# Kernel optimization log

Measured on AMD Instinct MI355X. Metric: run time of the kernel, lower is better.

The kernel has to match this reference:

```python
import jax, jax.numpy as jnp
import numpy as np

B, S, T = 1024, 1024, 16


def setup_inputs() -> dict:
    key = jax.random.key(0)
    k1, k2, k3, k4, k5 = jax.random.split(key, 5)
    emissions = jax.random.normal(k1, (B, S, T), dtype=jnp.float32)
    tags = jax.random.randint(k2, (B, S), 0, T, dtype=jnp.int64)
    mask = jnp.ones((B, S), dtype=bool)
    # parameters (original uses uniform(-0.1, 0.1) init)
    transitions = jax.random.uniform(k3, (T, T), minval=-0.1, maxval=0.1, dtype=jnp.float32)
    start_transitions = jax.random.uniform(k4, (T,), minval=-0.1, maxval=0.1, dtype=jnp.float32)
    end_transitions = jax.random.uniform(k5, (T,), minval=-0.1, maxval=0.1, dtype=jnp.float32)
    return {
        "emissions": emissions,
        "tags": tags,
        "mask": mask,
        "transitions": transitions,
        "start_transitions": start_transitions,
        "end_transitions": end_transitions,
    }


def _forward_algorithm(emissions, mask, transitions, start_transitions, end_transitions):
    # emissions: [B,S,T], mask: [B,S] bool -> log partition [B]
    score0 = start_transitions + emissions[:, 0]  # [B,T]

    def step(score, xs):
        em_t, m_t = xs  # em_t: [B,T], m_t: [B]
        # next[b,i,j] = score[b,i] + transitions[i,j] + em_t[b,j]
        nxt = score[:, :, None] + transitions[None, :, :] + em_t[:, None, :]
        nxt = jax.nn.logsumexp(nxt, axis=1)  # over previous tag i
        score = jnp.where(m_t[:, None], nxt, score)
        return score, None

    em_rest = jnp.swapaxes(emissions[:, 1:], 0, 1)  # [S-1,B,T]
    m_rest = jnp.swapaxes(mask[:, 1:], 0, 1)        # [S-1,B]
    score, _ = jax.lax.scan(step, score0, (em_rest, m_rest))
    score = score + end_transitions
    return jax.nn.logsumexp(score, axis=1)


def _score_sentence(emissions, tags, mask, transitions, start_transitions, end_transitions):
    # gold-path score, vectorized over time. [B]
    bidx = jnp.arange(emissions.shape[0])
    score = start_transitions[tags[:, 0]] + emissions[:, 0][bidx, tags[:, 0]]
    # per-step emission scores [B,S]
    emit = jnp.take_along_axis(emissions, tags[:, :, None], axis=2)[:, :, 0]
    # NOTE: faithful to original: transitions[tags[t], tags[t-1]]
    trans = transitions[tags[:, 1:], tags[:, :-1]]  # [B,S-1]
    m = mask[:, 1:].astype(emissions.dtype)
    score = score + jnp.sum((emit[:, 1:] + trans) * m, axis=1)
    last_idx = jnp.sum(mask.astype(jnp.int32), axis=1) - 1  # [B]
    last_tags = jnp.take_along_axis(tags, last_idx[:, None].astype(tags.dtype), axis=1)[:, 0]
    score = score + end_transitions[last_tags]
    return score


def reference(emissions, tags, mask, transitions, start_transitions, end_transitions):
    emissions = emissions.astype(jnp.float32)
    gold = _score_sentence(emissions, tags, mask, transitions, start_transitions, end_transitions)
    logZ = _forward_algorithm(emissions, mask, transitions, start_transitions, end_transitions)
    nll = logZ - gold
    return jnp.mean(nll)
```

## Files before the change

kernel.cpp:

```cpp
#include <hip/hip_runtime.h>
#include <stdint.h>


#define BB 1024
#define SS 1024
#define TT 16
#define WPB 8
#define TL  128
#define RS  16
#define MS  20
#define OFFLN2 3.29244911f

typedef float    f32x4 __attribute__((ext_vector_type(4)));
typedef float    f32x2 __attribute__((ext_vector_type(2)));
typedef int      i32x4 __attribute__((ext_vector_type(4)));
typedef short    s16x4 __attribute__((ext_vector_type(4)));
typedef uint32_t u32x2 __attribute__((ext_vector_type(2)));

__device__ __forceinline__ uint32_t pkt(float lo, float hi) {
    return __builtin_amdgcn_perm(__float_as_uint(hi), __float_as_uint(lo), 0x07060302u);
}
__device__ __forceinline__ s16x4 mk_frag(uint32_t lo, uint32_t hi) {
    u32x2 t; t.x = lo; t.y = hi;
    return __builtin_bit_cast(s16x4, t);
}

__global__ __launch_bounds__(512, 4) void crf_fused(
        const float* __restrict__ em,
        const float* __restrict__ trans,
        const int*   __restrict__ tags,
        const float* __restrict__ startt,
        const float* __restrict__ endt,
        float* __restrict__ part)
{
    __shared__ __align__(16) float xbuf[WPB][TL * RS];
    __shared__ __align__(16) int   scb [WPB][16];
    __shared__ float gpart[WPB];

    const int w    = threadIdx.x >> 6;
    const int lane = threadIdx.x & 63;
    const int b    = blockIdx.x;
    const int q    = lane >> 4;
    const int m    = lane & 15;

    const float comp = 1.00390625f;
    f32x2 e01, e23;
    e01.x = __expf(trans[(4*q + 0) * TT + m]) * comp;
    e01.y = __expf(trans[(4*q + 1) * TT + m]) * comp;
    e23.x = __expf(trans[(4*q + 2) * TT + m]) * comp;
    e23.y = __expf(trans[(4*q + 3) * TT + m]) * comp;
    const s16x4 eA = mk_frag(pkt(e01.x, e01.y), pkt(e23.x, e23.y));

    const float* ep = em + (size_t)b * SS * TT + (size_t)w * TL * TT + lane;
    float* xt = xbuf[w];
    #pragma unroll
    for (int h = 0; h < 2; ++h) {
        float v[16];
        #pragma unroll
        for (int k = 0; k < 16; ++k) v[k] = ep[(h * 16 + k) * 64];
        #pragma unroll
        for (int k = 0; k < 16; ++k) xt[(4 * (h * 16 + k) + q) * RS + m] = __expf(v[k] - OFFLN2);
    }

    {
        const int t0  = w * TL + lane;
        const int t1  = t0 + 64;
        const int tg0 = tags[b * SS + t0];
        const int tg1 = tags[b * SS + t1];
        float g0 = em[((size_t)b * SS + t0) * TT + tg0];
        float g1 = em[((size_t)b * SS + t1) * TT + tg1];
        g0 += (t0 > 0) ? trans[tg0 * TT + tags[b * SS + t0 - 1]] : startt[tg0];
        g1 += trans[tg1 * TT + tags[b * SS + t1 - 1]];
        if (t1 == SS - 1) g1 += endt[tg1];
        float gs = g0 + g1;
        #pragma unroll
        for (int s2 = 1; s2 < 64; s2 <<= 1) gs += __shfl_xor(gs, s2, 64);
        if (lane == 0) gpart[w] = gs;
    }

    f32x4 sd0, sd1;
    sd0[0] = sd1[0] = (4*q + 0 == m) ? 1.f : 0.f;
    sd0[1] = sd1[1] = (4*q + 1 == m) ? 1.f : 0.f;
    sd0[2] = sd1[2] = (4*q + 2 == m) ? 1.f : 0.f;
    sd0[3] = sd1[3] = (4*q + 3 == m) ? 1.f : 0.f;
    const f32x4 zero = {0.f, 0.f, 0.f, 0.f};
    const bool skip0 = (w == 0);

#define RESCALE(sd, sc) {                                                   \
        float mx = fmaxf(fmaxf(sd[0], sd[1]), fmaxf(sd[2], sd[3]));         \
        mx = fmaxf(mx, __shfl_xor(mx, 16, 64));                             \
        mx = fmaxf(mx, __shfl_xor(mx, 32, 64));                             \
        const int e_ = (int)(__float_as_uint(mx) >> 23) - 127;              \
        const float sf_ = __uint_as_float((uint32_t)(127 - e_) << 23);      \
        sd[0] *= sf_; sd[1] *= sf_; sd[2] *= sf_; sd[3] *= sf_;             \
        sc += e_; }

    const float* xr0 = xt + 4 * q;
    const float* xr1 = xt + 64 * RS + 4 * q;
    f32x4 c0[4], c1[4];
    #pragma unroll
    for (int i = 0; i < 4; ++i) {
        c0[i] = *(const f32x4*)(xr0 + i * RS);
        c1[i] = *(const f32x4*)(xr1 + i * RS);
    }

    #pragma unroll
    for (int g = 0; g < 16; ++g) {
        f32x4 n0[4], n1[4];
        if (g < 15) {
            #pragma unroll
            for (int i = 0; i < 4; ++i) {
                n0[i] = *(const f32x4*)(xr0 + (4 * (g + 1) + i) * RS);
                n1[i] = *(const f32x4*)(xr1 + (4 * (g + 1) + i) * RS);
            }
        }
        #pragma unroll
        for (int i = 0; i < 4; ++i) {
            if (!(skip0 && g == 0 && i == 0)) {
                const s16x4 b0 = mk_frag(pkt(sd0[0], sd0[1]), pkt(sd0[2], sd0[3]));
                sd0 = __builtin_amdgcn_mfma_f32_16x16x16bf16_1k(eA, b0, zero, 0, 0, 0);
                sd0 *= c0[i];
            }
            const s16x4 b1 = mk_frag(pkt(sd1[0], sd1[1]), pkt(sd1[2], sd1[3]));
            sd1 = __builtin_amdgcn_mfma_f32_16x16x16bf16_1k(eA, b1, zero, 0, 0, 0);
            sd1 *= c1[i];
        }
        #pragma unroll
        for (int i = 0; i < 4; ++i) { c0[i] = n0[i]; c1[i] = n1[i]; }
    }

    xt[(4*q + 0) * TT + m] = sd1[0];
    xt[(4*q + 1) * TT + m] = sd1[1];
    xt[(4*q + 2) * TT + m] = sd1[2];
    xt[(4*q + 3) * TT + m] = sd1[3];
    const f32x4 at = *(const f32x4*)(xt + m * TT + 4 * q);
    const s16x4 bfm = mk_frag(pkt(sd0[0], sd0[1]), pkt(sd0[2], sd0[3]));
    const s16x4 afm = mk_frag(pkt(at.x, at.y), pkt(at.z, at.w));
    f32x4 sdw = __builtin_amdgcn_mfma_f32_16x16x16bf16_1k(afm, bfm, zero, 0, 0, 0);
    int scw = 0;
    RESCALE(sdw, scw);

    xt[(4*q + 0) * MS + m] = sdw[0];
    xt[(4*q + 1) * MS + m] = sdw[1];
    xt[(4*q + 2) * MS + m] = sdw[2];
    xt[(4*q + 3) * MS + m] = sdw[3];
    if (q == 0) scb[w][m] = scw;
    __syncthreads();

    f32x4 d = zero; int sig = 0;
    #pragma unroll
    for (int lev = 0; lev < 3; ++lev) {
        const int nact = 4 >> lev;
        if (w < nact) {
            const int iA = (2 * w + 1) << lev;
            const int iB = (2 * w) << lev;
            const float* xA = xbuf[iA];
            float*       xB = xbuf[iB];
            const f32x4 a  = *(const f32x4*)(xA + m * MS + 4 * q);
            const i32x4 s4 = *(const i32x4*)(&scb[iA][4 * q]);
            const int   sB = scb[iB][m];
            int smax = max(max(s4.x, s4.y), max(s4.z, s4.w));
            smax = max(smax, __shfl_xor(smax, 16, 64));
            smax = max(smax, __shfl_xor(smax, 32, 64));
            const float bb0 = xB[(4*q + 0) * MS + m];
            const float bb1 = xB[(4*q + 1) * MS + m];
            const float bb2 = xB[(4*q + 2) * MS + m];
            const float bb3 = xB[(4*q + 3) * MS + m];
            const float u0 = ldexpf(bb0, s4.x - smax);
            const float u1 = ldexpf(bb1, s4.y - smax);
            const float u2 = ldexpf(bb2, s4.z - smax);
            const float u3 = ldexpf(bb3, s4.w - smax);
            const s16x4 bfr = mk_frag(pkt(u0, u1), pkt(u2, u3));
            const s16x4 afr = mk_frag(pkt(a.x, a.y), pkt(a.z, a.w));
            f32x4 dd = __builtin_amdgcn_mfma_f32_16x16x16bf16_1k(afr, bfr, zero, 0, 0, 0);
            int sc_ = sB + smax;
            RESCALE(dd, sc_);
            if (lev == 2) { d = dd; sig = sc_; }
            else {
                xB[(4*q + 0) * MS + m] = dd[0];
                xB[(4*q + 1) * MS + m] = dd[1];
                xB[(4*q + 2) * MS + m] = dd[2];
                xB[(4*q + 3) * MS + m] = dd[3];
                if (q == 0) scb[iB][m] = sc_;
            }
        }
        if (lev < 2) __syncthreads();
    }
#undef RESCALE

    if (w == 0) {
        const float s0 = startt[m] + em[(size_t)b * SS * TT + m];
        float mx0 = s0;
        #pragma unroll
        for (int s2 = 1; s2 < 16; s2 <<= 1) mx0 = fmaxf(mx0, __shfl_xor(mx0, s2, 64));
        const float u0n = __expf(s0 - mx0);
        int sigmax = sig;
        #pragma unroll
        for (int s2 = 1; s2 < 16; s2 <<= 1) sigmax = max(sigmax, __shfl_xor(sigmax, s2, 64));
        const float wt = ldexpf(u0n, sig - sigmax);
        f32x4 v;
        v[0] = d[0] * wt; v[1] = d[1] * wt; v[2] = d[2] * wt; v[3] = d[3] * wt;
        #pragma unroll
        for (int s2 = 1; s2 < 16; s2 <<= 1) {
            v[0] += __shfl_xor(v[0], s2, 64);
            v[1] += __shfl_xor(v[1], s2, 64);
            v[2] += __shfl_xor(v[2], s2, 64);
            v[3] += __shfl_xor(v[3], s2, 64);
        }
        const f32x4 ee = *(const f32x4*)(endt + 4 * q);
        float z = __expf(ee.x) * v[0] + __expf(ee.y) * v[1]
                + __expf(ee.z) * v[2] + __expf(ee.w) * v[3];
        z += __shfl_xor(z, 16, 64);
        z += __shfl_xor(z, 32, 64);
        if (lane == 0) {
            float gb = 0.f;
            #pragma unroll
            for (int i = 0; i < WPB; ++i) gb += gpart[i];
            part[b] = mx0 + 0.69314718055994531f * (float)sigmax
                    + 1023.0f * OFFLN2 + __logf(z) - gb;
        }
    }
}

__global__ __launch_bounds__(256) void reduce_kernel(const float* __restrict__ part,
                                                     float* __restrict__ out)
{
    __shared__ float red[256];
    const int tid = threadIdx.x;
    float s = 0.f;
    #pragma unroll
    for (int i = 0; i < 4; ++i) s += part[tid + 256 * i];
    red[tid] = s;
    __syncthreads();
    for (int k = 128; k > 0; k >>= 1) {
        if (tid < k) red[tid] += red[tid + k];
        __syncthreads();
    }
    if (tid == 0) out[0] = red[0] * (1.0f / BB);
}

extern "C" void kernel_launch(void* const* d_in, const int* in_sizes, int n_in,
                              void* d_out, int out_size, void* d_ws, size_t ws_size,
                              hipStream_t stream) {
    const float* em     = (const float*)d_in[0];
    const int*   tags   = (const int*)  d_in[1];
    const float* trans  = (const float*)d_in[3];
    const float* startt = (const float*)d_in[4];
    const float* endt   = (const float*)d_in[5];
    float* out  = (float*)d_out;
    float* part = (float*)d_ws;

    crf_fused<<<BB, 512, 0, stream>>>(em, trans, tags, startt, endt, part);
    reduce_kernel<<<1, 256, 0, stream>>>(part, out);
}
```

Before: 120.8 us.

## Split chain into two halves with smaller LDS tile and fold emission into A operand

Each wave now processes its 128-step segment as two 64-step halves, reusing a smaller transposed LDS buffer (16x68 floats instead of 128x16). This cuts LDS per block and raises the launch bound to 8 blocks per CU. Emissions are folded into the A operand (exp(trans) scaled by exp(emission)), which removes the post-MFMA vector multiply. MFMAs switch to the 16x16x32 bf16 instruction with the upper half zero-padded. The trade-off is more A-operand packing per step, a serialized second load phase between the halves, and an extra combining MFMA.

```diff
diff --git a/kernel.cpp b/kernel.cpp
--- a/kernel.cpp
+++ b/kernel.cpp
@@ -7,25 +7,89 @@
 #define TT 16
 #define WPB 8
 #define TL  128
-#define RS  16
+#define XS  68
 #define MS  20
 #define OFFLN2 3.29244911f
 
 typedef float    f32x4 __attribute__((ext_vector_type(4)));
 typedef float    f32x2 __attribute__((ext_vector_type(2)));
 typedef int      i32x4 __attribute__((ext_vector_type(4)));
-typedef short    s16x4 __attribute__((ext_vector_type(4)));
-typedef uint32_t u32x2 __attribute__((ext_vector_type(2)));
+typedef short    s16x8 __attribute__((ext_vector_type(8)));
+typedef uint32_t u32x4 __attribute__((ext_vector_type(4)));
 
 __device__ __forceinline__ uint32_t pkt(float lo, float hi) {
     return __builtin_amdgcn_perm(__float_as_uint(hi), __float_as_uint(lo), 0x07060302u);
 }
-__device__ __forceinline__ s16x4 mk_frag(uint32_t lo, uint32_t hi) {
-    u32x2 t; t.x = lo; t.y = hi;
-    return __builtin_bit_cast(s16x4, t);
-}
-
-__global__ __launch_bounds__(512, 4) void crf_fused(
+
+#define RESCALE(sd, sc) {                                                   \
+        float mx_ = fmaxf(fmaxf(sd[0], sd[1]), fmaxf(sd[2], sd[3]));        \
+        mx_ = fmaxf(mx_, __shfl_xor(mx_, 16, 64));                          \
+        mx_ = fmaxf(mx_, __shfl_xor(mx_, 32, 64));                          \
+        const int e_ = (int)(__float_as_uint(mx_) >> 23) - 127;             \
+        const float sf_ = __uint_as_float((uint32_t)(127 - e_) << 23);      \
+        sd[0] *= sf_; sd[1] *= sf_; sd[2] *= sf_; sd[3] *= sf_;             \
+        sc += e_; }
+
+__device__ __forceinline__ void run_chains(float* xt, const f32x2 e01, const f32x2 e23,
+                                           const int q, const int m, const bool skip_first,
+                                           f32x4& P, int& sc)
+{
+    const f32x4 zero = {0.f, 0.f, 0.f, 0.f};
+    f32x4 sd0, sd1;
+    sd0[0] = sd1[0] = (4*q + 0 == m) ? 1.f : 0.f;
+    sd0[1] = sd1[1] = (4*q + 1 == m) ? 1.f : 0.f;
+    sd0[2] = sd1[2] = (4*q + 2 == m) ? 1.f : 0.f;
+    sd0[3] = sd1[3] = (4*q + 3 == m) ? 1.f : 0.f;
+    u32x4 au0, au1, bu0, bu1;
+    au0.z = au0.w = au1.z = au1.w = 0u;
+    bu0.z = bu0.w = bu1.z = bu1.w = 0u;
+
+    const float* xr0 = xt + m * XS;
+    const float* xr1 = xr0 + 32;
+
+    #pragma unroll
+    for (int g = 0; g < 8; ++g) {
+        const f32x4 c0 = *(const f32x4*)(xr0 + 4 * g);
+        const f32x4 c1 = *(const f32x4*)(xr1 + 4 * g);
+        #pragma unroll
+        for (int i = 0; i < 4; ++i) {
+            if (!(skip_first && g == 0 && i == 0)) {
+                f32x2 xx; xx.x = c0[i]; xx.y = c0[i];
+                const f32x2 a01 = xx * e01;
+                const f32x2 a23 = xx * e23;
+                au0.x = pkt(a01.x, a01.y); au0.y = pkt(a23.x, a23.y);
+                bu0.x = pkt(sd0[0], sd0[1]); bu0.y = pkt(sd0[2], sd0[3]);
+                sd0 = __builtin_amdgcn_mfma_f32_16x16x32_bf16(
+                        __builtin_bit_cast(s16x8, au0), __builtin_bit_cast(s16x8, bu0),
+                        zero, 0, 0, 0);
+            }
+            {
+                f32x2 xx; xx.x = c1[i]; xx.y = c1[i];
+                const f32x2 a01 = xx * e01;
+                const f32x2 a23 = xx * e23;
+                au1.x = pkt(a01.x, a01.y); au1.y = pkt(a23.x, a23.y);
+                bu1.x = pkt(sd1[0], sd1[1]); bu1.y = pkt(sd1[2], sd1[3]);
+                sd1 = __builtin_amdgcn_mfma_f32_16x16x32_bf16(
+                        __builtin_bit_cast(s16x8, au1), __builtin_bit_cast(s16x8, bu1),
+                        zero, 0, 0, 0);
+            }
+        }
+    }
+
+    xt[(4*q + 0) * TT + m] = sd1[0];
+    xt[(4*q + 1) * TT + m] = sd1[1];
+    xt[(4*q + 2) * TT + m] = sd1[2];
+    xt[(4*q + 3) * TT + m] = sd1[3];
+    const f32x4 at = *(const f32x4*)(xt + m * TT + 4 * q);
+    au0.x = pkt(at.x, at.y);   au0.y = pkt(at.z, at.w);
+    bu0.x = pkt(sd0[0], sd0[1]); bu0.y = pkt(sd0[2], sd0[3]);
+    P = __builtin_amdgcn_mfma_f32_16x16x32_bf16(
+            __builtin_bit_cast(s16x8, au0), __builtin_bit_cast(s16x8, bu0), zero, 0, 0, 0);
+    sc = 0;
+    RESCALE(P, sc);
+}
+
+__global__ __launch_bounds__(512, 8) void crf_fused(
         const float* __restrict__ em,
         const float* __restrict__ trans,
         const int*   __restrict__ tags,
@@ -33,7 +97,7 @@
         const float* __restrict__ endt,
         float* __restrict__ part)
 {
-    __shared__ __align__(16) float xbuf[WPB][TL * RS];
+    __shared__ __align__(16) float xbuf[WPB][TT * XS];
     __shared__ __align__(16) int   scb [WPB][16];
     __shared__ float gpart[WPB];
 
@@ -49,17 +113,16 @@
     e01.y = __expf(trans[(4*q + 1) * TT + m]) * comp;
     e23.x = __expf(trans[(4*q + 2) * TT + m]) * comp;
     e23.y = __expf(trans[(4*q + 3) * TT + m]) * comp;
-    const s16x4 eA = mk_frag(pkt(e01.x, e01.y), pkt(e23.x, e23.y));
-
+
+    float* xt = xbuf[w];
     const float* ep = em + (size_t)b * SS * TT + (size_t)w * TL * TT + lane;
-    float* xt = xbuf[w];
-    #pragma unroll
-    for (int h = 0; h < 2; ++h) {
+
+    {
         float v[16];
         #pragma unroll
-        for (int k = 0; k < 16; ++k) v[k] = ep[(h * 16 + k) * 64];
-        #pragma unroll
-        for (int k = 0; k < 16; ++k) xt[(4 * (h * 16 + k) + q) * RS + m] = __expf(v[k] - OFFLN2);
+        for (int k = 0; k < 16; ++k) v[k] = ep[k * 64];
+        #pragma unroll
+        for (int k = 0; k < 16; ++k) xt[m * XS + 4 * k + q] = __expf(v[k] - OFFLN2);
     }
 
     {
@@ -78,66 +141,32 @@
         if (lane == 0) gpart[w] = gs;
     }
 
-    f32x4 sd0, sd1;
-    sd0[0] = sd1[0] = (4*q + 0 == m) ? 1.f : 0.f;
-    sd0[1] = sd1[1] = (4*q + 1 == m) ? 1.f : 0.f;
-    sd0[2] = sd1[2] = (4*q + 2 == m) ? 1.f : 0.f;
-    sd0[3] = sd1[3] = (4*q + 3 == m) ? 1.f : 0.f;
+    f32x4 PA; int scA;
+    run_chains(xt, e01, e23, q, m, (w == 0), PA, scA);
+
+    {
+        float v[16];
+        #pragma unroll
+        for (int k = 0; k < 16; ++k) v[k] = ep[(16 + k) * 64];
+        #pragma unroll
+        for (int k = 0; k < 16; ++k) xt[m * XS + 4 * k + q] = __expf(v[k] - OFFLN2);
+    }
+    f32x4 PB; int scB;
+    run_chains(xt, e01, e23, q, m, false, PB, scB);
+
     const f32x4 zero = {0.f, 0.f, 0.f, 0.f};
-    const bool skip0 = (w == 0);
-
-#define RESCALE(sd, sc) {                                                   \
-        float mx = fmaxf(fmaxf(sd[0], sd[1]), fmaxf(sd[2], sd[3]));         \
-        mx = fmaxf(mx, __shfl_xor(mx, 16, 64));                             \
-        mx = fmaxf(mx, __shfl_xor(mx, 32, 64));                             \
-        const int e_ = (int)(__float_as_uint(mx) >> 23) - 127;              \
-        const float sf_ = __uint_as_float((uint32_t)(127 - e_) << 23);      \
-        sd[0] *= sf_; sd[1] *= sf_; sd[2] *= sf_; sd[3] *= sf_;             \
-        sc += e_; }
-
-    const float* xr0 = xt + 4 * q;
-    const float* xr1 = xt + 64 * RS + 4 * q;
-    f32x4 c0[4], c1[4];
-    #pragma unroll
-    for (int i = 0; i < 4; ++i) {
-        c0[i] = *(const f32x4*)(xr0 + i * RS);
-        c1[i] = *(const f32x4*)(xr1 + i * RS);
-    }
-
-    #pragma unroll
-    for (int g = 0; g < 16; ++g) {
-        f32x4 n0[4], n1[4];
-        if (g < 15) {
-            #pragma unroll
-            for (int i = 0; i < 4; ++i) {
-                n0[i] = *(const f32x4*)(xr0 + (4 * (g + 1) + i) * RS);
-                n1[i] = *(const f32x4*)(xr1 + (4 * (g + 1) + i) * RS);
-            }
-        }
-        #pragma unroll
-        for (int i = 0; i < 4; ++i) {
-            if (!(skip0 && g == 0 && i == 0)) {
-                const s16x4 b0 = mk_frag(pkt(sd0[0], sd0[1]), pkt(sd0[2], sd0[3]));
-                sd0 = __builtin_amdgcn_mfma_f32_16x16x16bf16_1k(eA, b0, zero, 0, 0, 0);
-                sd0 *= c0[i];
-            }
-            const s16x4 b1 = mk_frag(pkt(sd1[0], sd1[1]), pkt(sd1[2], sd1[3]));
-            sd1 = __builtin_amdgcn_mfma_f32_16x16x16bf16_1k(eA, b1, zero, 0, 0, 0);
-            sd1 *= c1[i];
-        }
-        #pragma unroll
-        for (int i = 0; i < 4; ++i) { c0[i] = n0[i]; c1[i] = n1[i]; }
-    }
-
-    xt[(4*q + 0) * TT + m] = sd1[0];
-    xt[(4*q + 1) * TT + m] = sd1[1];
-    xt[(4*q + 2) * TT + m] = sd1[2];
-    xt[(4*q + 3) * TT + m] = sd1[3];
+    xt[(4*q + 0) * TT + m] = PB[0];
+    xt[(4*q + 1) * TT + m] = PB[1];
+    xt[(4*q + 2) * TT + m] = PB[2];
+    xt[(4*q + 3) * TT + m] = PB[3];
     const f32x4 at = *(const f32x4*)(xt + m * TT + 4 * q);
-    const s16x4 bfm = mk_frag(pkt(sd0[0], sd0[1]), pkt(sd0[2], sd0[3]));
-    const s16x4 afm = mk_frag(pkt(at.x, at.y), pkt(at.z, at.w));
-    f32x4 sdw = __builtin_amdgcn_mfma_f32_16x16x16bf16_1k(afm, bfm, zero, 0, 0, 0);
-    int scw = 0;
+    u32x4 au, bu;
+    au.z = au.w = bu.z = bu.w = 0u;
+    au.x = pkt(at.x, at.y);   au.y = pkt(at.z, at.w);
+    bu.x = pkt(PA[0], PA[1]); bu.y = pkt(PA[2], PA[3]);
+    f32x4 sdw = __builtin_amdgcn_mfma_f32_16x16x32_bf16(
+            __builtin_bit_cast(s16x8, au), __builtin_bit_cast(s16x8, bu), zero, 0, 0, 0);
+    int scw = scA + scB;
     RESCALE(sdw, scw);
 
     xt[(4*q + 0) * MS + m] = sdw[0];
@@ -170,9 +199,12 @@
             const float u1 = ldexpf(bb1, s4.y - smax);
             const float u2 = ldexpf(bb2, s4.z - smax);
             const float u3 = ldexpf(bb3, s4.w - smax);
-            const s16x4 bfr = mk_frag(pkt(u0, u1), pkt(u2, u3));
-            const s16x4 afr = mk_frag(pkt(a.x, a.y), pkt(a.z, a.w));
-            f32x4 dd = __builtin_amdgcn_mfma_f32_16x16x16bf16_1k(afr, bfr, zero, 0, 0, 0);
+            u32x4 ta, tb;
+            ta.z = ta.w = tb.z = tb.w = 0u;
+            ta.x = pkt(a.x, a.y); ta.y = pkt(a.z, a.w);
+            tb.x = pkt(u0, u1);   tb.y = pkt(u2, u3);
+            f32x4 dd = __builtin_amdgcn_mfma_f32_16x16x32_bf16(
+                    __builtin_bit_cast(s16x8, ta), __builtin_bit_cast(s16x8, tb), zero, 0, 0, 0);
             int sc_ = sB + smax;
             RESCALE(dd, sc_);
             if (lev == 2) { d = dd; sig = sc_; }
@@ -186,7 +218,6 @@
         }
         if (lev < 2) __syncthreads();
     }
-#undef RESCALE
 
     if (w == 0) {
         const float s0 = startt[m] + em[(size_t)b * SS * TT + m];
```

Result: slower. 125.9 us (+4.2%).
